# Performance work log

Hardware: AMD Instinct MI355X
Metric: run time of the kernel (lower is better)

The kernel has to match this reference:

```python
import jax, jax.numpy as jnp
import numpy as np

S = 64          # image_size / sdf cube side / embed dim
P = 4           # frame & sdf patch size
NC = 4          # number_of_couples
HP = 8          # num_heads
E = 32          # embedding_middle_attention
FC = 4          # final_number_of_channels
G = S // P      # 16 patches per side
N_FR = G * G * NC      # 1024 frame tokens
N_SDF = G ** 3         # 4096 sdf tokens
N = N_FR + N_SDF       # 5120 total tokens
NB = N // S            # 80 blocks


def setup_inputs() -> dict:
    key = jax.random.key(0)
    ks = jax.random.split(key, 12)
    s = 0.05  # keep attention logits numerically sane
    return {
        "cond1": jax.random.normal(ks[0], (1, 1, S, S, S), jnp.float32),
        "cond2": jax.random.uniform(ks[1], (1, 1, 4 * NC, S, S), jnp.float32),
        "W_emb": jax.random.normal(ks[2], (S, P * P * 4), jnp.float32) * s,   # Linear weight (out,in)
        "b_emb": jnp.zeros((S,), jnp.float32),
        "W_conv3d": jax.random.normal(ks[3], (S, 1, P, P, P), jnp.float32) * s,
        "b_conv3d": jnp.zeros((S,), jnp.float32),
        "pos_emb": jax.random.normal(ks[4], (N, S), jnp.float32) * s,
        "WQ": jax.random.normal(ks[5], (HP, S, E), jnp.float32) * s,
        "WK": jax.random.normal(ks[6], (HP, S, E), jnp.float32) * s,
        "WV": jax.random.normal(ks[7], (HP, S, E), jnp.float32) * s,
        "W_out": jax.random.normal(ks[8], (HP * E, S), jnp.float32) * s,
        "ln_gamma": jnp.ones((N, S), jnp.float32),
        "ln_beta": jnp.zeros((N, S), jnp.float32),
        "W_conv2d": jax.random.normal(ks[9], (S * FC, NB), jnp.float32) * s,  # 1x1 conv (out,in)
        "b_conv2d": jnp.zeros((S * FC,), jnp.float32),
    }


def _frames_to_patches(frames, W_emb, b_emb):
    # frames: (B,1,C,H,W) with C=4*NC, H=W=S
    b = frames.shape[0]
    x = frames[:, 0]                       # (B,C,S,S)
    x = x.transpose(0, 2, 3, 1)            # (B,S,S,C)
    x = x.reshape(b, G, P, G, P, 4 * NC)
    x = x.transpose(0, 1, 3, 2, 4, 5)      # (B,G,G,P,P,C)
    x = x.reshape(b, G * G, P, P, 4 * NC)
    x = x.transpose(0, 1, 4, 2, 3)         # (B,Np,C,P,P)
    # tensor_split along channels into NC chunks, cat along token dim
    x = x.reshape(b, G * G, NC, 4, P, P).transpose(0, 2, 1, 3, 4, 5)
    x = x.reshape(b, N_FR, 4 * P * P)      # flatten (c,i,j) row-major, matches torch
    return x @ W_emb.T + b_emb             # (B, N_FR, S)


def _sdf_to_patches(sdf, W_conv3d, b_conv3d):
    # Conv3d with kernel==stride==P is exact non-overlapping patching + matmul
    b = sdf.shape[0]
    x = sdf[:, 0]                                       # (B,S,S,S)
    x = x.reshape(b, G, P, G, P, G, P)
    x = x.transpose(0, 1, 3, 5, 2, 4, 6)                # (B,G,G,G,P,P,P)
    x = x.reshape(b, N_SDF, P ** 3)
    wc = W_conv3d.reshape(S, P ** 3)                    # (out, d*h*w), same flatten order
    return x @ wc.T + b_conv3d                          # (B, N_SDF, S)


def reference(cond1, cond2, W_emb, b_emb, W_conv3d, b_conv3d, pos_emb,
              WQ, WK, WV, W_out, ln_gamma, ln_beta, W_conv2d, b_conv2d):
    b = cond1.shape[0]
    fr = _frames_to_patches(cond2, W_emb, b_emb)        # (B,1024,64)
    sd = _sdf_to_patches(cond1, W_conv3d, b_conv3d)     # (B,4096,64)
    X = jnp.concatenate([sd, fr], axis=1) + pos_emb     # (B,N,64)

    # manual multi-head attention
    Q = jnp.einsum('bnd,hde->bhne', X, WQ)
    K = jnp.einsum('bnd,hde->bhne', X, WK)
    V = jnp.einsum('bnd,hde->bhne', X, WV)
    scores = jnp.einsum('bhne,bhme->bhnm', Q, K) / jnp.sqrt(jnp.float32(E))
    A = jax.nn.softmax(scores, axis=-1)
    O = jnp.einsum('bhnm,bhme->bhne', A, V)             # (B,H,N,E)
    O = O.transpose(0, 2, 1, 3).reshape(b, N, HP * E)   # head-order concat
    Xn = O @ W_out + X                                  # residual

    # LayerNorm over BOTH (N, emb) axes (torch LayerNorm((N,S)))
    mu = jnp.mean(Xn, axis=(1, 2), keepdims=True)
    var = jnp.mean(jnp.square(Xn - mu), axis=(1, 2), keepdims=True)
    Xn = (Xn - mu) / jnp.sqrt(var + 1e-5) * ln_gamma + ln_beta

    # adapt: reshape to blocks, 1x1 conv2d, reshape to volume
    Xr = Xn.reshape(b, NB, S, S)
    Xc = jnp.einsum('bchw,oc->bohw', Xr, W_conv2d) + b_conv2d[None, :, None, None]
    return Xc.reshape(b, FC, S, S, S)
```

## Files before the change

### kernel.cpp

```cpp
#include <hip/hip_runtime.h>
#include <hip/hip_bf16.h>

typedef short bf16x8 __attribute__((ext_vector_type(8)));
typedef float f32x4 __attribute__((ext_vector_type(4)));
typedef unsigned short u16;
typedef unsigned int u32;

#define NTOK 5120
#define NSDF 4096

__device__ __forceinline__ float b2f(u16 x){
  u32 u = ((u32)x) << 16; float f; __builtin_memcpy(&f, &u, 4); return f;
}
__device__ __forceinline__ u16 f2b(float f){
  u32 u; __builtin_memcpy(&u, &f, 4);
  return (u16)((u + 0x7fffu + ((u >> 16) & 1u)) >> 16);
}
__device__ __forceinline__ u32 cvtpk(float lo, float hi){
  u32 r;
  asm("v_cvt_pk_bf16_f32 %0, %1, %2" : "=v"(r) : "v"(lo), "v"(hi));
  return r;
}
__device__ __forceinline__ f32x4 mfma16(bf16x8 a, bf16x8 b, f32x4 c){
  return __builtin_amdgcn_mfma_f32_16x16x32_bf16(a, b, c, 0, 0, 0);
}
__device__ __forceinline__ void gld16(const void* g, void* l){
  __builtin_amdgcn_global_load_lds(
      (const __attribute__((address_space(1))) u32*)g,
      (__attribute__((address_space(3))) u32*)l, 16, 0, 0);
}

__global__ __launch_bounds__(256) void k_prep(
    const float* __restrict__ WQ, const float* __restrict__ WK, const float* __restrict__ WV,
    const float* __restrict__ W_out, const float* __restrict__ W_emb,
    const float* __restrict__ W_c3, const float* __restrict__ Wc,
    u16* __restrict__ Wt, u16* __restrict__ Wto, u16* __restrict__ Wemb_b,
    u16* __restrict__ Wc3_b, u16* __restrict__ Wcb)
{
  int gid = blockIdx.x * 256 + threadIdx.x;
  int gsz = gridDim.x * 256;
  for (int i = gid; i < 49152; i += gsz){
    int m = i >> 14, r = i & 16383;
    int h = r >> 11, d = (r >> 5) & 63, e = r & 31;
    const float* src = (m == 0) ? WQ : ((m == 1) ? WK : WV);
    float v = src[(h * 64 + d) * 32 + e];
    if (m == 0) v *= 0.17677669529663689f * 1.4426950408889634f;
    Wt[((m * 8 + h) * 32 + e) * 64 + d] = f2b(v);
  }
  for (int i = gid; i < 16384; i += gsz){
    int k = i >> 6, d = i & 63;
    Wto[d * 256 + k] = f2b(W_out[i]);
  }
  for (int i = gid; i < 4096; i += gsz) Wemb_b[i] = f2b(W_emb[i]);
  for (int i = gid; i < 4096; i += gsz) Wc3_b[i] = f2b(W_c3[i]);
  for (int i = gid; i < 20480; i += gsz) Wcb[i] = f2b(Wc[i]);
}

__global__ __launch_bounds__(256) void k_build_x(
    const float* __restrict__ cond1, const float* __restrict__ cond2,
    const u16* __restrict__ Wemb_b, const float* __restrict__ b_emb,
    const u16* __restrict__ Wc3_b, const float* __restrict__ b_c3,
    const float* __restrict__ pos, u16* __restrict__ Xout)
{
  __shared__ __align__(16) u16 Psh[64][72];
  int b = blockIdx.x, t = threadIdx.x;
  bool sdb = (b < 64);
  {
    int nl = t >> 2, sub = t & 3;
    const float* src = sdb ? cond1 : cond2;
    int nn = sdb ? (b * 64 + nl) : (b * 64 + nl - NSDF);
    int g0 = nn >> 8, g1 = (nn >> 4) & 15, g2 = nn & 15;
    const float* sp = src + (g0 * 4 + sub) * 4096 + g1 * 4 * 64 + g2 * 4;
    for (int p1 = 0; p1 < 4; ++p1){
      float4 v = *(const float4*)(sp + p1 * 64);
      ushort4 o;
      o.x = f2b(v.x); o.y = f2b(v.y); o.z = f2b(v.z); o.w = f2b(v.w);
      *(ushort4*)&Psh[nl][sub * 16 + p1 * 4] = o;
    }
  }
  __syncthreads();
  int w = t >> 6, lane = t & 63, l15 = lane & 15, g = lane >> 4;
  const u16* Wm = sdb ? Wc3_b : Wemb_b;
  const float* bias = sdb ? b_c3 : b_emb;
  bf16x8 a0 = *(const bf16x8*)&Psh[w * 16 + l15][g * 8];
  bf16x8 a1 = *(const bf16x8*)&Psh[w * 16 + l15][32 + g * 8];
  for (int nb = 0; nb < 4; ++nb){
    bf16x8 b0 = *(const bf16x8*)(Wm + (nb * 16 + l15) * 64 + g * 8);
    bf16x8 b1 = *(const bf16x8*)(Wm + (nb * 16 + l15) * 64 + 32 + g * 8);
    f32x4 acc = {0.f, 0.f, 0.f, 0.f};
    acc = mfma16(a0, b0, acc);
    acc = mfma16(a1, b1, acc);
    int d = nb * 16 + l15;
    float bs = bias[d];
    for (int r = 0; r < 4; ++r){
      int tok = b * 64 + w * 16 + g * 4 + r;
      float v = acc[r] + bs + pos[tok * 64 + d];
      Xout[tok * 64 + d] = f2b(v);
    }
  }
}

__global__ __launch_bounds__(256) void k_qkv(
    const u16* __restrict__ X, const u16* __restrict__ Wt,
    u16* __restrict__ Q, u16* __restrict__ K, u16* __restrict__ VT)
{
  __shared__ __align__(16) u16 Xsh[64][72];
  int bid = blockIdx.x, b = bid / 6, grp = bid % 6;
  int t = threadIdx.x;
  {
    int nl = t >> 2, cb = t & 3;
    const u16* sp = X + (b * 64 + nl) * 64 + cb * 16;
    *(bf16x8*)&Xsh[nl][cb * 16] = *(const bf16x8*)(sp);
    *(bf16x8*)&Xsh[nl][cb * 16 + 8] = *(const bf16x8*)(sp + 8);
  }
  __syncthreads();
  int w = t >> 6, lane = t & 63, l15 = lane & 15, g = lane >> 4;
  int pair = grp * 4 + w, m = pair >> 3, h = pair & 7;
  bf16x8 a0[4], a1[4];
  for (int ms = 0; ms < 4; ++ms){
    a0[ms] = *(const bf16x8*)&Xsh[ms * 16 + l15][g * 8];
    a1[ms] = *(const bf16x8*)&Xsh[ms * 16 + l15][32 + g * 8];
  }
  for (int nb = 0; nb < 2; ++nb){
    const u16* wp = Wt + ((m * 8 + h) * 32 + nb * 16 + l15) * 64;
    bf16x8 b0 = *(const bf16x8*)(wp + g * 8);
    bf16x8 b1 = *(const bf16x8*)(wp + 32 + g * 8);
    int e = nb * 16 + l15;
    for (int ms = 0; ms < 4; ++ms){
      f32x4 acc = {0.f, 0.f, 0.f, 0.f};
      acc = mfma16(a0[ms], b0, acc);
      acc = mfma16(a1[ms], b1, acc);
      for (int r = 0; r < 4; ++r){
        int n = b * 64 + ms * 16 + g * 4 + r;
        u16 v = f2b(acc[r]);
        if (m == 0)      Q[(h * NTOK + n) * 32 + e] = v;
        else if (m == 1) K[(h * NTOK + n) * 32 + e] = v;
        else             VT[(h * 32 + e) * NTOK + n] = v;
      }
    }
  }
}

__global__ __launch_bounds__(256) void k_attn(
    const u16* __restrict__ Q, const u16* __restrict__ K, const u16* __restrict__ VT,
    u16* __restrict__ Opb, float* __restrict__ lpart)
{
  __shared__ __align__(16) u16 Ksh[2][128 * 32];
  __shared__ __align__(16) u16 Vsh[2][32 * 128];
  int bid = blockIdx.x;
  int x = bid & 7;
  int inner = bid >> 3;
  int qb = inner % 40;
  int p = x + 8 * (inner / 40);
  int sp = p >> 3, h = p & 7;
  int t = threadIdx.x, w = t >> 6, lane = t & 63, l15 = lane & 15, g = lane >> 4;
  int q0w = qb * 128 + w * 32;
  int kb = sp * 1280;
  int wb = w * 512;

  int rho0 = t >> 2, cpK = t & 3;
  int key0 = (rho0 & 0x60) | ((rho0 & 0x0C) << 1) | ((rho0 & 0x10) >> 2) | (rho0 & 3);
  int clogK = cpK ^ (rho0 & 3);
  const uint4* kg0 = (const uint4*)(K + (size_t)(h * NTOK + kb + key0) * 32 + clogK * 8);
  const uint4* kg1 = (const uint4*)(K + (size_t)(h * NTOK + kb + key0 + 64) * 32 + clogK * 8);
  int eV = t >> 4, cpV = t & 15;
  int clogV = cpV ^ eV;
  const uint4* vg0 = (const uint4*)(VT + (size_t)(h * 32 + eV) * NTOK + kb + clogV * 8);
  const uint4* vg1 = (const uint4*)(VT + (size_t)(h * 32 + eV + 16) * NTOK + kb + clogV * 8);

  bf16x8 qf0 = *(const bf16x8*)(Q + (size_t)(h * NTOK + q0w + l15) * 32 + g * 8);
  bf16x8 qf1 = *(const bf16x8*)(Q + (size_t)(h * NTOK + q0w + 16 + l15) * 32 + g * 8);

  union { u16 s[8]; bf16x8 v; } one8;
  #pragma unroll
  for (int j = 0; j < 8; ++j) one8.s[j] = 0x3F80;
  bf16x8 ones = one8.v;

  f32x4 oc[2][2];
  for (int u = 0; u < 2; ++u) for (int eb = 0; eb < 2; ++eb) oc[u][eb] = (f32x4){0.f,0.f,0.f,0.f};
  f32x4 als0 = {0.f,0.f,0.f,0.f}, als1 = {0.f,0.f,0.f,0.f};

  int kf_base = l15 * 32 + ((g ^ (l15 & 3)) * 8);

  gld16(kg0, &Ksh[0][wb]);
  gld16(kg1, &Ksh[0][wb + 2048]);
  gld16(vg0, &Vsh[0][wb]);
  gld16(vg1, &Vsh[0][wb + 2048]);

  for (int kt = 0; kt < 10; ++kt){
    int cur = kt & 1, nxt = cur ^ 1;
    if (kt < 9){
      gld16(kg0 + (kt + 1) * 512, &Ksh[nxt][wb]);
      gld16(kg1 + (kt + 1) * 512, &Ksh[nxt][wb + 2048]);
      gld16(vg0 + (kt + 1) * 16,  &Vsh[nxt][wb]);
      gld16(vg1 + (kt + 1) * 16,  &Vsh[nxt][wb + 2048]);
      asm volatile("s_waitcnt vmcnt(4)" ::: "memory");
    } else {
      asm volatile("s_waitcnt vmcnt(0)" ::: "memory");
    }
    __builtin_amdgcn_sched_barrier(0);
    __builtin_amdgcn_s_barrier();
    __builtin_amdgcn_sched_barrier(0);
    const u16* kB = &Ksh[cur][0];
    const u16* vB = &Vsh[cur][0];
    #pragma unroll
    for (int ks = 0; ks < 4; ++ks){
      f32x4 z = {0.f,0.f,0.f,0.f};
      bf16x8 kf0 = *(const bf16x8*)(kB + kf_base + ks * 1024);
      bf16x8 kf1 = *(const bf16x8*)(kB + kf_base + ks * 1024 + 512);
      f32x4 s0a = mfma16(kf0, qf0, z);
      f32x4 s1a = mfma16(kf1, qf0, z);
      f32x4 s0b = mfma16(kf0, qf1, z);
      f32x4 s1b = mfma16(kf1, qf1, z);
      int vf_off = l15 * 128 + (((ks * 4 + g) ^ l15) * 8);
      bf16x8 vf0 = *(const bf16x8*)(vB + vf_off);
      bf16x8 vf1 = *(const bf16x8*)(vB + vf_off + 2048);
      float pa0 = __builtin_amdgcn_exp2f(s0a[0]);
      float pa1 = __builtin_amdgcn_exp2f(s0a[1]);
      float pa2 = __builtin_amdgcn_exp2f(s0a[2]);
      float pa3 = __builtin_amdgcn_exp2f(s0a[3]);
      float pa4 = __builtin_amdgcn_exp2f(s1a[0]);
      float pa5 = __builtin_amdgcn_exp2f(s1a[1]);
      float pa6 = __builtin_amdgcn_exp2f(s1a[2]);
      float pa7 = __builtin_amdgcn_exp2f(s1a[3]);
      union { bf16x8 v; u32 wd[4]; } pua;
      pua.wd[0] = cvtpk(pa0, pa1); pua.wd[1] = cvtpk(pa2, pa3);
      pua.wd[2] = cvtpk(pa4, pa5); pua.wd[3] = cvtpk(pa6, pa7);
      float pb0 = __builtin_amdgcn_exp2f(s0b[0]);
      float pb1 = __builtin_amdgcn_exp2f(s0b[1]);
      float pb2 = __builtin_amdgcn_exp2f(s0b[2]);
      float pb3 = __builtin_amdgcn_exp2f(s0b[3]);
      float pb4 = __builtin_amdgcn_exp2f(s1b[0]);
      float pb5 = __builtin_amdgcn_exp2f(s1b[1]);
      float pb6 = __builtin_amdgcn_exp2f(s1b[2]);
      float pb7 = __builtin_amdgcn_exp2f(s1b[3]);
      union { bf16x8 v; u32 wd[4]; } pub;
      pub.wd[0] = cvtpk(pb0, pb1); pub.wd[1] = cvtpk(pb2, pb3);
      pub.wd[2] = cvtpk(pb4, pb5); pub.wd[3] = cvtpk(pb6, pb7);
      oc[0][0] = mfma16(pua.v, vf0, oc[0][0]);
      oc[0][1] = mfma16(pua.v, vf1, oc[0][1]);
      oc[1][0] = mfma16(pub.v, vf0, oc[1][0]);
      oc[1][1] = mfma16(pub.v, vf1, oc[1][1]);
      als0 = mfma16(pua.v, ones, als0);
      als1 = mfma16(pub.v, ones, als1);
    }
    __builtin_amdgcn_sched_barrier(0);
    __builtin_amdgcn_s_barrier();
  }

  u16* opp = Opb + ((size_t)(sp * 8 + h) * NTOK + q0w) * 32;
  for (int u = 0; u < 2; ++u)
    for (int eb = 0; eb < 2; ++eb)
      for (int r = 0; r < 4; ++r)
        opp[(u * 16 + 4 * g + r) * 32 + eb * 16 + l15] = f2b(oc[u][eb][r]);
  if (l15 == 0){
    float* lp = lpart + (size_t)(sp * 8 + h) * NTOK + q0w;
    #pragma unroll
    for (int r = 0; r < 4; ++r){
      lp[4 * g + r]      = als0[r];
      lp[16 + 4 * g + r] = als1[r];
    }
  }
}

__global__ __launch_bounds__(64) void k_xn(
    const u16* __restrict__ Opb, const float* __restrict__ lpart,
    const u16* __restrict__ Wto, const u16* __restrict__ X,
    float* __restrict__ Xn, float* __restrict__ partials)
{
  int b = blockIdx.x, lane = threadIdx.x, l15 = lane & 15, g = lane >> 4;
  int n0 = b * 16;
  int n = n0 + l15;
  f32x4 acc[4];
  #pragma unroll
  for (int nb = 0; nb < 4; ++nb) acc[nb] = (f32x4){0.f,0.f,0.f,0.f};
  #pragma unroll
  for (int ks = 0; ks < 8; ++ks){
    float l = lpart[(size_t)(0 * 8 + ks) * NTOK + n]
            + lpart[(size_t)(1 * 8 + ks) * NTOK + n]
            + lpart[(size_t)(2 * 8 + ks) * NTOK + n]
            + lpart[(size_t)(3 * 8 + ks) * NTOK + n];
    float rl = 1.0f / l;
    float ac0 = 0.f, ac1 = 0.f, ac2 = 0.f, ac3 = 0.f;
    float ac4 = 0.f, ac5 = 0.f, ac6 = 0.f, ac7 = 0.f;
    #pragma unroll
    for (int sp = 0; sp < 4; ++sp){
      union { bf16x8 v; u16 s[8]; } u;
      u.v = *(const bf16x8*)(Opb + (((size_t)(sp * 8 + ks) * NTOK + n) << 5) + g * 8);
      ac0 += b2f(u.s[0]); ac1 += b2f(u.s[1]); ac2 += b2f(u.s[2]); ac3 += b2f(u.s[3]);
      ac4 += b2f(u.s[4]); ac5 += b2f(u.s[5]); ac6 += b2f(u.s[6]); ac7 += b2f(u.s[7]);
    }
    union { bf16x8 v; u32 wd[4]; } m;
    m.wd[0] = cvtpk(ac0 * rl, ac1 * rl);
    m.wd[1] = cvtpk(ac2 * rl, ac3 * rl);
    m.wd[2] = cvtpk(ac4 * rl, ac5 * rl);
    m.wd[3] = cvtpk(ac6 * rl, ac7 * rl);
    bf16x8 av = m.v;
    #pragma unroll
    for (int nb = 0; nb < 4; ++nb){
      bf16x8 bb = *(const bf16x8*)(Wto + (nb * 16 + l15) * 256 + ks * 32 + g * 8);
      acc[nb] = mfma16(av, bb, acc[nb]);
    }
  }
  float s1 = 0.f, s2 = 0.f;
  #pragma unroll
  for (int nb = 0; nb < 4; ++nb){
    int d = nb * 16 + l15;
    #pragma unroll
    for (int r = 0; r < 4; ++r){
      int nn = n0 + g * 4 + r;
      float v = acc[nb][r] + b2f(X[nn * 64 + d]);
      Xn[nn * 64 + d] = v;
      s1 += v; s2 += v * v;
    }
  }
  for (int off = 1; off < 64; off <<= 1){
    s1 += __shfl_xor(s1, off);
    s2 += __shfl_xor(s2, off);
  }
  if (lane == 0){
    partials[b * 2]     = s1;
    partials[b * 2 + 1] = s2;
  }
}

__global__ __launch_bounds__(256) void k_out(
    const float* __restrict__ Xn, const float* __restrict__ partials,
    const float* __restrict__ gamma, const float* __restrict__ beta,
    const u16* __restrict__ Wcb, const float* __restrict__ bc,
    float* __restrict__ out)
{
  __shared__ float redA[8];
  __shared__ float murs2[2];
  __shared__ __align__(16) float Xs[80 * 16];
  int bid = blockIdx.x, t = threadIdx.x, w = t >> 6, lane = t & 63;
  int hh = bid >> 2, wq = (bid & 3) * 16;
  float s1 = 0.f, s2 = 0.f;
  for (int i = t; i < 320; i += 256){
    s1 += partials[2 * i];
    s2 += partials[2 * i + 1];
  }
  for (int off = 1; off < 64; off <<= 1){ s1 += __shfl_xor(s1, off); s2 += __shfl_xor(s2, off); }
  if (lane == 0){ redA[w * 2] = s1; redA[w * 2 + 1] = s2; }
  __syncthreads();
  if (t == 0){
    float S1 = redA[0] + redA[2] + redA[4] + redA[6];
    float S2 = redA[1] + redA[3] + redA[5] + redA[7];
    const float inv = 1.0f / 327680.0f;
    float mu = S1 * inv;
    murs2[0] = mu;
    murs2[1] = rsqrtf(S2 * inv - mu * mu + 1e-5f);
  }
  __syncthreads();
  float mu = murs2[0], rs = murs2[1];
  for (int i = t; i < 1280; i += 256){
    int c = i >> 4, ww = wq + (i & 15);
    int idx = (c * 64 + hh) * 64 + ww;
    Xs[i] = (Xn[idx] - mu) * rs * gamma[idx] + beta[idx];
  }
  __syncthreads();
  int o = t;
  const u16* wr = Wcb + o * 80;
  f32x4 acc4[4];
  for (int k = 0; k < 4; ++k) acc4[k] = (f32x4){0.f,0.f,0.f,0.f};
  for (int c = 0; c < 80; ++c){
    float wt = b2f(wr[c]);
    for (int k = 0; k < 4; ++k)
      acc4[k] += (*(const f32x4*)&Xs[c * 16 + k * 4]) * wt;
  }
  float bb = bc[o];
  for (int k = 0; k < 4; ++k)
    for (int j = 0; j < 4; ++j)
      out[o * 4096 + hh * 64 + wq + k * 4 + j] = acc4[k][j] + bb;
}

extern "C" void kernel_launch(void* const* d_in, const int* in_sizes, int n_in,
                              void* d_out, int out_size, void* d_ws, size_t ws_size,
                              hipStream_t stream) {
  const float* cond1 = (const float*)d_in[0];
  const float* cond2 = (const float*)d_in[1];
  const float* W_emb = (const float*)d_in[2];
  const float* b_emb = (const float*)d_in[3];
  const float* W_c3  = (const float*)d_in[4];
  const float* b_c3  = (const float*)d_in[5];
  const float* pos   = (const float*)d_in[6];
  const float* WQ    = (const float*)d_in[7];
  const float* WK    = (const float*)d_in[8];
  const float* WV    = (const float*)d_in[9];
  const float* W_out = (const float*)d_in[10];
  const float* gamma = (const float*)d_in[11];
  const float* beta  = (const float*)d_in[12];
  const float* Wc    = (const float*)d_in[13];
  const float* bc    = (const float*)d_in[14];
  float* out = (float*)d_out;
  char* ws = (char*)d_ws;

  u16*   X   = (u16*)(ws);
  u16*   Q   = (u16*)(ws +   655360);
  u16*   Kq  = (u16*)(ws +  3276800);
  u16*   VT  = (u16*)(ws +  5898240);
  float* Xn  = (float*)(ws + 11141120);
  u16*   Wt  = (u16*)(ws + 12451840);
  u16*   Wto = (u16*)(ws + 12550144);
  float* partials = (float*)(ws + 12582912);
  u16*   Wemb_b = (u16*)(ws + 12585472);
  u16*   Wc3_b  = (u16*)(ws + 12593664);
  u16*   Wcb    = (u16*)(ws + 12601856);
  u16*   Opb    = (u16*)(ws + 12648448);
  float* lpart  = (float*)(ws + 23134208);

  k_prep<<<32, 256, 0, stream>>>(WQ, WK, WV, W_out, W_emb, W_c3, Wc,
                                 Wt, Wto, Wemb_b, Wc3_b, Wcb);
  k_build_x<<<80, 256, 0, stream>>>(cond1, cond2, Wemb_b, b_emb, Wc3_b, b_c3, pos, X);
  k_qkv<<<480, 256, 0, stream>>>(X, Wt, Q, Kq, VT);
  k_attn<<<1280, 256, 0, stream>>>(Q, Kq, VT, Opb, lpart);
  k_xn<<<320, 64, 0, stream>>>(Opb, lpart, Wto, X, Xn, partials);
  k_out<<<256, 256, 0, stream>>>(Xn, partials, gamma, beta, Wcb, bc, out);
}
```

Before: 81.59 us.

## Fold weight prep into build_x launch and stage V transpose through LDS

Removes the separate k_prep launch. Extra blocks of k_build_x now convert the QKV, output and conv2d weights, and the embedding and conv3d weights are converted per block into shared memory. In k_qkv, the V-projection blocks write their results into LDS first and then store VT with coalesced 16-byte row writes, replacing the scattered 2-byte strided stores. This saves one kernel launch and the uncoalesced VT writes, at the cost of each build_x block redundantly converting a 4096-element weight and one extra barrier in the V path.

```diff
diff --git a/kernel.cpp b/kernel.cpp
--- a/kernel.cpp
+++ b/kernel.cpp
@@ -30,40 +30,37 @@
       (__attribute__((address_space(3))) u32*)l, 16, 0, 0);
 }
 
-__global__ __launch_bounds__(256) void k_prep(
-    const float* __restrict__ WQ, const float* __restrict__ WK, const float* __restrict__ WV,
-    const float* __restrict__ W_out, const float* __restrict__ W_emb,
-    const float* __restrict__ W_c3, const float* __restrict__ Wc,
-    u16* __restrict__ Wt, u16* __restrict__ Wto, u16* __restrict__ Wemb_b,
-    u16* __restrict__ Wc3_b, u16* __restrict__ Wcb)
-{
-  int gid = blockIdx.x * 256 + threadIdx.x;
-  int gsz = gridDim.x * 256;
-  for (int i = gid; i < 49152; i += gsz){
-    int m = i >> 14, r = i & 16383;
-    int h = r >> 11, d = (r >> 5) & 63, e = r & 31;
-    const float* src = (m == 0) ? WQ : ((m == 1) ? WK : WV);
-    float v = src[(h * 64 + d) * 32 + e];
-    if (m == 0) v *= 0.17677669529663689f * 1.4426950408889634f;
-    Wt[((m * 8 + h) * 32 + e) * 64 + d] = f2b(v);
-  }
-  for (int i = gid; i < 16384; i += gsz){
-    int k = i >> 6, d = i & 63;
-    Wto[d * 256 + k] = f2b(W_out[i]);
-  }
-  for (int i = gid; i < 4096; i += gsz) Wemb_b[i] = f2b(W_emb[i]);
-  for (int i = gid; i < 4096; i += gsz) Wc3_b[i] = f2b(W_c3[i]);
-  for (int i = gid; i < 20480; i += gsz) Wcb[i] = f2b(Wc[i]);
-}
-
 __global__ __launch_bounds__(256) void k_build_x(
     const float* __restrict__ cond1, const float* __restrict__ cond2,
-    const u16* __restrict__ Wemb_b, const float* __restrict__ b_emb,
-    const u16* __restrict__ Wc3_b, const float* __restrict__ b_c3,
-    const float* __restrict__ pos, u16* __restrict__ Xout)
+    const float* __restrict__ W_emb, const float* __restrict__ b_emb,
+    const float* __restrict__ W_c3, const float* __restrict__ b_c3,
+    const float* __restrict__ pos, u16* __restrict__ Xout,
+    const float* __restrict__ WQ, const float* __restrict__ WK,
+    const float* __restrict__ WV, const float* __restrict__ W_out,
+    const float* __restrict__ Wc,
+    u16* __restrict__ Wt, u16* __restrict__ Wto, u16* __restrict__ Wcb)
 {
   __shared__ __align__(16) u16 Psh[64][72];
+  __shared__ __align__(16) u16 Wsh[64][72];
   int b = blockIdx.x, t = threadIdx.x;
+  if (b >= 80){
+    int gid = (b - 80) * 256 + t;
+    const int gsz = 32 * 256;
+    for (int i = gid; i < 49152; i += gsz){
+      int m = i >> 14, r = i & 16383;
+      int h = r >> 11, d = (r >> 5) & 63, e = r & 31;
+      const float* src = (m == 0) ? WQ : ((m == 1) ? WK : WV);
+      float v = src[(h * 64 + d) * 32 + e];
+      if (m == 0) v *= 0.17677669529663689f * 1.4426950408889634f;
+      Wt[((m * 8 + h) * 32 + e) * 64 + d] = f2b(v);
+    }
+    for (int i = gid; i < 16384; i += gsz){
+      int k = i >> 6, d = i & 63;
+      Wto[d * 256 + k] = f2b(W_out[i]);
+    }
+    for (int i = gid; i < 20480; i += gsz) Wcb[i] = f2b(Wc[i]);
+    return;
+  }
   bool sdb = (b < 64);
   {
     int nl = t >> 2, sub = t & 3;
@@ -78,15 +75,19 @@
       *(ushort4*)&Psh[nl][sub * 16 + p1 * 4] = o;
     }
   }
+  {
+    const float* Wf = sdb ? W_c3 : W_emb;
+    for (int i = t; i < 4096; i += 256)
+      Wsh[i >> 6][i & 63] = f2b(Wf[i]);
+  }
   __syncthreads();
   int w = t >> 6, lane = t & 63, l15 = lane & 15, g = lane >> 4;
-  const u16* Wm = sdb ? Wc3_b : Wemb_b;
   const float* bias = sdb ? b_c3 : b_emb;
   bf16x8 a0 = *(const bf16x8*)&Psh[w * 16 + l15][g * 8];
   bf16x8 a1 = *(const bf16x8*)&Psh[w * 16 + l15][32 + g * 8];
   for (int nb = 0; nb < 4; ++nb){
-    bf16x8 b0 = *(const bf16x8*)(Wm + (nb * 16 + l15) * 64 + g * 8);
-    bf16x8 b1 = *(const bf16x8*)(Wm + (nb * 16 + l15) * 64 + 32 + g * 8);
+    bf16x8 b0 = *(const bf16x8*)&Wsh[nb * 16 + l15][g * 8];
+    bf16x8 b1 = *(const bf16x8*)&Wsh[nb * 16 + l15][32 + g * 8];
     f32x4 acc = {0.f, 0.f, 0.f, 0.f};
     acc = mfma16(a0, b0, acc);
     acc = mfma16(a1, b1, acc);
@@ -105,6 +106,7 @@
     u16* __restrict__ Q, u16* __restrict__ K, u16* __restrict__ VT)
 {
   __shared__ __align__(16) u16 Xsh[64][72];
+  __shared__ __align__(16) u16 Vsh[4][32][72];
   int bid = blockIdx.x, b = bid / 6, grp = bid % 6;
   int t = threadIdx.x;
   {
@@ -121,23 +123,46 @@
     a0[ms] = *(const bf16x8*)&Xsh[ms * 16 + l15][g * 8];
     a1[ms] = *(const bf16x8*)&Xsh[ms * 16 + l15][32 + g * 8];
   }
-  for (int nb = 0; nb < 2; ++nb){
-    const u16* wp = Wt + ((m * 8 + h) * 32 + nb * 16 + l15) * 64;
-    bf16x8 b0 = *(const bf16x8*)(wp + g * 8);
-    bf16x8 b1 = *(const bf16x8*)(wp + 32 + g * 8);
-    int e = nb * 16 + l15;
-    for (int ms = 0; ms < 4; ++ms){
-      f32x4 acc = {0.f, 0.f, 0.f, 0.f};
-      acc = mfma16(a0[ms], b0, acc);
-      acc = mfma16(a1[ms], b1, acc);
-      for (int r = 0; r < 4; ++r){
-        int n = b * 64 + ms * 16 + g * 4 + r;
-        u16 v = f2b(acc[r]);
-        if (m == 0)      Q[(h * NTOK + n) * 32 + e] = v;
-        else if (m == 1) K[(h * NTOK + n) * 32 + e] = v;
-        else             VT[(h * 32 + e) * NTOK + n] = v;
+  if (grp < 4){
+    for (int nb = 0; nb < 2; ++nb){
+      const u16* wp = Wt + ((m * 8 + h) * 32 + nb * 16 + l15) * 64;
+      bf16x8 b0 = *(const bf16x8*)(wp + g * 8);
+      bf16x8 b1 = *(const bf16x8*)(wp + 32 + g * 8);
+      int e = nb * 16 + l15;
+      for (int ms = 0; ms < 4; ++ms){
+        f32x4 acc = {0.f, 0.f, 0.f, 0.f};
+        acc = mfma16(a0[ms], b0, acc);
+        acc = mfma16(a1[ms], b1, acc);
+        for (int r = 0; r < 4; ++r){
+          int n = b * 64 + ms * 16 + g * 4 + r;
+          u16 v = f2b(acc[r]);
+          if (m == 0) Q[(h * NTOK + n) * 32 + e] = v;
+          else        K[(h * NTOK + n) * 32 + e] = v;
+        }
       }
     }
+  } else {
+    for (int nb = 0; nb < 2; ++nb){
+      const u16* wp = Wt + ((2 * 8 + h) * 32 + nb * 16 + l15) * 64;
+      bf16x8 b0 = *(const bf16x8*)(wp + g * 8);
+      bf16x8 b1 = *(const bf16x8*)(wp + 32 + g * 8);
+      int e = nb * 16 + l15;
+      for (int ms = 0; ms < 4; ++ms){
+        f32x4 acc = {0.f, 0.f, 0.f, 0.f};
+        acc = mfma16(a0[ms], b0, acc);
+        acc = mfma16(a1[ms], b1, acc);
+        for (int r = 0; r < 4; ++r)
+          Vsh[w][e][ms * 16 + g * 4 + r] = f2b(acc[r]);
+      }
+    }
+    __syncthreads();
+    int hl = t >> 6, e = (t >> 1) & 31, part = t & 1;
+    int hglob = (grp - 4) * 4 + hl;
+    const u16* src = &Vsh[hl][e][part * 32];
+    u16* dst = VT + (size_t)(hglob * 32 + e) * NTOK + b * 64 + part * 32;
+    #pragma unroll
+    for (int j = 0; j < 4; ++j)
+      *(uint4*)(dst + j * 8) = *(const uint4*)(src + j * 8);
   }
 }
 
@@ -403,15 +428,12 @@
   u16*   Wt  = (u16*)(ws + 12451840);
   u16*   Wto = (u16*)(ws + 12550144);
   float* partials = (float*)(ws + 12582912);
-  u16*   Wemb_b = (u16*)(ws + 12585472);
-  u16*   Wc3_b  = (u16*)(ws + 12593664);
   u16*   Wcb    = (u16*)(ws + 12601856);
   u16*   Opb    = (u16*)(ws + 12648448);
   float* lpart  = (float*)(ws + 23134208);
 
-  k_prep<<<32, 256, 0, stream>>>(WQ, WK, WV, W_out, W_emb, W_c3, Wc,
-                                 Wt, Wto, Wemb_b, Wc3_b, Wcb);
-  k_build_x<<<80, 256, 0, stream>>>(cond1, cond2, Wemb_b, b_emb, Wc3_b, b_c3, pos, X);
+  k_build_x<<<112, 256, 0, stream>>>(cond1, cond2, W_emb, b_emb, W_c3, b_c3, pos, X,
+                                     WQ, WK, WV, W_out, Wc, Wt, Wto, Wcb);
   k_qkv<<<480, 256, 0, stream>>>(X, Wt, Q, Kq, VT);
   k_attn<<<1280, 256, 0, stream>>>(Q, Kq, VT, Opb, lpart);
   k_xn<<<320, 64, 0, stream>>>(Opb, lpart, Wto, X, Xn, partials);
```

Measured after the change: 73.76 us. 9.6% less time.
